# Performance work log

Measured on AMD Instinct MI355X. Metric: run time of the kernel, lower is better.

The kernel has to match this reference:

```python
import jax, jax.numpy as jnp
import numpy as np

N, CIN, C, COUT, K27, KNN_K = 65536, 1, 128, 128, 27, 16
C4, C2 = C // 4, C // 2


def _w(key, shape, fan_in):
    return (jax.random.normal(key, shape, dtype=jnp.float32) * (fan_in ** -0.5))


def setup_inputs() -> dict:
    key = jax.random.key(0)
    ks = jax.random.split(key, 32)
    inp = {
        "feats": jax.random.normal(ks[0], (N, CIN), dtype=jnp.float32),
        # kernel-map neighbor indices; value N means 'no neighbor at this offset'
        "nbr_idx": jax.random.randint(ks[1], (N, K27), 0, N + 1, dtype=jnp.int32),
        "knn_idx": jax.random.randint(ks[2], (N, KNN_K), 0, N, dtype=jnp.int32),
        "W_in": _w(ks[3], (K27, CIN, C), K27 * CIN), "b_in": jnp.zeros((C,), jnp.float32),
        "W_conv0": _w(ks[4], (3, K27, C, C), K27 * C), "b_conv0": jnp.zeros((3, C), jnp.float32),
        "W_conv1": _w(ks[5], (3, K27, C, C), K27 * C), "b_conv1": jnp.zeros((3, C), jnp.float32),
        "Wq": _w(ks[6], (3, C, C), C), "Wk": _w(ks[7], (3, C, C), C),
        "Wv": _w(ks[8], (3, C, C), C), "Wo": _w(ks[9], (3, C, C), C),
        "bo": jnp.zeros((3, C), jnp.float32),
        "W_a0": _w(ks[10], (3, C, C4), C), "b_a0": jnp.zeros((3, C4), jnp.float32),
        "W_a1": _w(ks[11], (3, K27, C4, C4), K27 * C4), "b_a1": jnp.zeros((3, C4), jnp.float32),
        "W_a2": _w(ks[12], (3, C4, C2), C4), "b_a2": jnp.zeros((3, C2), jnp.float32),
        "W_b0": _w(ks[13], (3, K27, C, C4), K27 * C), "b_b0": jnp.zeros((3, C4), jnp.float32),
        "W_b1": _w(ks[14], (3, K27, C4, C2), K27 * C4), "b_b1": jnp.zeros((3, C2), jnp.float32),
        "W_out": _w(ks[15], (K27, C, COUT), K27 * C), "b_out": jnp.zeros((COUT,), jnp.float32),
    }
    return inp


def sparse_conv(x, idx, W, b):
    # x: [N,Cin]; idx: [N,27] with pad value N -> zero feature
    xp = jnp.concatenate([x, jnp.zeros((1, x.shape[1]), x.dtype)], axis=0)
    g = xp[idx]  # [N,27,Cin]
    return jnp.einsum('nkc,kco->no', g, W) + b


def knn_attn(x, idx, Wq, Wk, Wv, Wo, bo):
    q = x @ Wq
    kf = x @ Wk
    vf = x @ Wv
    kn = kf[idx]  # [N,k,C]
    vn = vf[idx]
    logits = jnp.einsum('nc,nkc->nk', q, kn) * (x.shape[-1] ** -0.5)
    a = jax.nn.softmax(logits, axis=-1)
    agg = jnp.einsum('nk,nkc->nc', a, vn)
    return x + agg @ Wo + bo


def irn(x, idx, Wa0, ba0, Wa1, ba1, Wa2, ba2, Wb0, bb0, Wb1, bb1):
    r = jax.nn.relu
    h = r(x @ Wa0 + ba0)                      # 1x1 conv
    h = r(sparse_conv(h, idx, Wa1, ba1))       # 3x3x3
    out0 = r(h @ Wa2 + ba2)                    # 1x1 conv
    g = r(sparse_conv(x, idx, Wb0, bb0))
    out1 = r(sparse_conv(g, idx, Wb1, bb1))
    return jnp.concatenate([out0, out1], axis=-1) + x


def reference(feats, nbr_idx, knn_idx, W_in, b_in, W_conv0, b_conv0, W_conv1, b_conv1,
              Wq, Wk, Wv, Wo, bo, W_a0, b_a0, W_a1, b_a1, W_a2, b_a2,
              W_b0, b_b0, W_b1, b_b1, W_out, b_out):
    r = jax.nn.relu
    out = sparse_conv(feats, nbr_idx, W_in, b_in)
    for s in range(3):
        h = sparse_conv(out, nbr_idx, W_conv0[s], b_conv0[s])
        h = r(knn_attn(h, knn_idx, Wq[s], Wk[s], Wv[s], Wo[s], bo[s]))
        h = sparse_conv(h, nbr_idx, W_conv1[s], b_conv1[s])
        out = irn(h, nbr_idx, W_a0[s], b_a0[s], W_a1[s], b_a1[s], W_a2[s], b_a2[s],
                  W_b0[s], b_b0[s], W_b1[s], b_b1[s])
    return sparse_conv(out, nbr_idx, W_out, b_out)
```

## Files before the change

kernel.cpp:

```cpp
#include <hip/hip_runtime.h>
#include <stdint.h>

typedef unsigned short u16;
typedef __attribute__((ext_vector_type(8))) short bf16x8;
typedef __attribute__((ext_vector_type(4))) float f32x4;

#define NPTS 65536
#define NK27 27
#define KNN 16

__device__ __forceinline__ u16 f2b(float f) {
  union { float f; uint32_t u; } v; v.f = f;
  uint32_t r = (v.u + 0x7fffu + ((v.u >> 16) & 1u)) >> 16;
  return (u16)r;
}
__device__ __forceinline__ float b2f(u16 h) {
  union { uint32_t u; float f; } v; v.u = ((uint32_t)h) << 16; return v.f;
}

__global__ __launch_bounds__(256) void wtrans(const float* __restrict__ src, u16* __restrict__ dst,
                                              int G, int CI, int CO) {
  int id = blockIdx.x * 256 + threadIdx.x;
  int tot = G * CI * CO;
  if (id >= tot) return;
  int cpr = CI / 8;
  int swzb = (cpr < 8 ? cpr : 8) - 1;
  int g = id / (CI * CO);
  int r = id - g * (CI * CO);
  int co = r / CI;
  int cis = r - co * CI;
  int c = cis / 8, e = cis - c * 8;
  int ci = (c ^ (co & swzb)) * 8 + e;
  dst[id] = f2b(src[(size_t)g * CI * CO + (size_t)ci * CO + co]);
}

__global__ __launch_bounds__(256) void itrans(const int* __restrict__ nbr, int* __restrict__ out) {
  int id = blockIdx.x * 256 + threadIdx.x;
  int k = id >> 16;
  int n = id & (NPTS - 1);
  out[id] = nbr[n * NK27 + k];
}

__global__ void zero_pads(u16* a, u16* b, u16* c, u16* d, u16* e) {
  int t = threadIdx.x;
  if (t < 128) { a[t] = 0; b[t] = 0; c[t] = 0; }
  if (t < 32) { d[t] = 0; e[t] = 0; }
}

__global__ __launch_bounds__(256) void conv_in_k(const float* __restrict__ feats, const int* __restrict__ idx,
                                                 const float* __restrict__ W, const float* __restrict__ b,
                                                 u16* __restrict__ out) {
  int t = blockIdx.x * 256 + threadIdx.x;
  int n = t >> 7;
  int co = t & 127;
  float acc = b[co];
  for (int k = 0; k < NK27; ++k) {
    int m = idx[n * NK27 + k];
    float f = (m < NPTS) ? feats[m] : 0.0f;
    acc += f * W[k * 128 + co];
  }
  out[(size_t)n * 128 + co] = f2b(acc);
}

#define GLDS16(g, l)                                                                        \
  __builtin_amdgcn_global_load_lds((const __attribute__((address_space(1))) void*)(g),      \
                                   (__attribute__((address_space(3))) void*)(l), 16, 0, 0)

template<int CIN, int COUT, int NK, int EMODE, bool OUTF32>
__global__ __launch_bounds__(512, 2)
void sconv(const u16* __restrict__ x, const int* __restrict__ idxt,
           const u16* __restrict__ Wt, const float* __restrict__ bias,
           const u16* __restrict__ res, int res_stride,
           void* __restrict__ yout, int out_stride) {
  static_assert(NK == 1 || (NK & 1), "NK odd or 1");
  constexpr int BM = 256;
  constexpr int KK = CIN / 32;
  constexpr int CPR = CIN / 8;
  constexpr int SWZB = (CPR < 8 ? CPR : 8) - 1;
  constexpr int N_REP = COUT / 16;
  constexpr int M_REP = 2;
  constexpr int BSZ = COUT * CIN;
  constexpr int BCH = BSZ / 8;
  constexpr int BISS = (BCH + 511) / 512;

  __shared__ __attribute__((aligned(16))) u16 Bs[2][BSZ];

  const int tid = threadIdx.x;
  const int lane = tid & 63;
  const int wave = tid >> 6;
  const int n0 = blockIdx.x * BM;
  const int lr = lane & 15;
  const int lh = lane >> 4;
  const int row0 = wave * 32;

  f32x4 acc[M_REP][N_REP];
#pragma unroll
  for (int i = 0; i < M_REP; ++i)
#pragma unroll
    for (int j = 0; j < N_REP; ++j) acc[i][j] = (f32x4){0.f, 0.f, 0.f, 0.f};

  bf16x8 A0[M_REP][KK], A1[M_REP][KK];
  int mn[M_REP];

  auto stageB = [&](int k) {
    const u16* src = Wt + (size_t)k * BSZ;
    u16* dst = &Bs[k & 1][0];
#pragma unroll
    for (int i = 0; i < BISS; ++i) {
      int cb = i * 512 + wave * 64;
      if (BCH % 512 == 0 || cb < BCH)
        GLDS16(src + (size_t)(cb + lane) * 8, dst + (size_t)cb * 8);
    }
  };
  auto loadIdx = [&](int k, int (&m)[M_REP]) {
#pragma unroll
    for (int mr = 0; mr < M_REP; ++mr)
      m[mr] = idxt[(size_t)k * NPTS + n0 + row0 + mr * 16 + lr];
  };
  auto issueA = [&](const int (&m)[M_REP], bf16x8 (&dst)[M_REP][KK]) {
#pragma unroll
    for (int mr = 0; mr < M_REP; ++mr)
#pragma unroll
      for (int kk = 0; kk < KK; ++kk)
        dst[mr][kk] = *(const bf16x8*)(x + (size_t)m[mr] * CIN + kk * 32 + lh * 8);
  };
  auto compute = [&](int buf, const bf16x8 (&AR)[M_REP][KK]) {
#pragma unroll
    for (int kk = 0; kk < KK; ++kk) {
      bf16x8 b[N_REP];
      int pc = (kk * 4 + lh) ^ (lr & SWZB);
#pragma unroll
      for (int nr = 0; nr < N_REP; ++nr)
        b[nr] = *(const bf16x8*)(&Bs[buf][(nr * 16 + lr) * CIN + pc * 8]);
#pragma unroll
      for (int mr = 0; mr < M_REP; ++mr)
#pragma unroll
        for (int nr = 0; nr < N_REP; ++nr)
          acc[mr][nr] = __builtin_amdgcn_mfma_f32_16x16x32_bf16(AR[mr][kk], b[nr], acc[mr][nr], 0, 0, 0);
    }
  };

  {
    int m0[M_REP];
    if (NK == 1) {
#pragma unroll
      for (int mr = 0; mr < M_REP; ++mr) m0[mr] = n0 + row0 + mr * 16 + lr;
    } else {
      loadIdx(0, m0);
    }
    stageB(0);
    issueA(m0, A0);
    if (NK > 1) loadIdx(1, mn);
  }
  __syncthreads();

#define TAP(kv, AR, AW)                                                       \
  {                                                                           \
    const int k_ = (kv);                                                      \
    if (k_ + 1 < NK) {                                                        \
      stageB(k_ + 1);                                                         \
      issueA(mn, AW);                                                         \
      if (k_ + 2 < NK) loadIdx(k_ + 2, mn);                                   \
    }                                                                         \
    __builtin_amdgcn_sched_barrier(0);                                        \
    compute(k_ & 1, AR);                                                      \
    if (k_ + 1 < NK) __syncthreads();                                         \
  }

  if constexpr (NK == 1) {
    compute(0, A0);
  } else {
    int k = 0;
    for (; k + 2 < NK; k += 2) {
      TAP(k, A0, A1);
      TAP(k + 1, A1, A0);
    }
    TAP(k, A0, A1);
  }
#undef TAP

#pragma unroll
  for (int mr = 0; mr < M_REP; ++mr) {
#pragma unroll
    for (int nr = 0; nr < N_REP; ++nr) {
      int col = nr * 16 + lr;
      float bv = bias ? bias[col] : 0.0f;
#pragma unroll
      for (int j = 0; j < 4; ++j) {
        int n = n0 + row0 + mr * 16 + lh * 4 + j;
        float v = acc[mr][nr][j] + bv;
        if (EMODE == 1) v = fmaxf(v, 0.0f);
        else if (EMODE == 2) v = fmaxf(v + b2f(res[(size_t)n * res_stride + col]), 0.0f);
        else if (EMODE == 3) v = fmaxf(v, 0.0f) + b2f(res[(size_t)n * res_stride + col]);
        if (OUTF32) ((float*)yout)[(size_t)n * out_stride + col] = v;
        else ((u16*)yout)[(size_t)n * out_stride + col] = f2b(v);
      }
    }
  }
}

__global__ __launch_bounds__(256)
void attn_k(const u16* __restrict__ qb, const u16* __restrict__ kb,
            const u16* __restrict__ vb, const int* __restrict__ knn,
            u16* __restrict__ agg) {
  int n = (blockIdx.x * 256 + threadIdx.x) >> 6;
  int lane = threadIdx.x & 63;
  int c0 = lane * 2;
  uint32_t qp = *(const uint32_t*)(qb + (size_t)n * 128 + c0);
  float q0 = b2f((u16)(qp & 0xffff)), q1 = b2f((u16)(qp >> 16));
  float lg[KNN];
  int ms[KNN];
#pragma unroll
  for (int j = 0; j < KNN; ++j) {
    int m = knn[n * KNN + j];
    ms[j] = m;
    uint32_t kp = *(const uint32_t*)(kb + (size_t)m * 128 + c0);
    float p = q0 * b2f((u16)(kp & 0xffff)) + q1 * b2f((u16)(kp >> 16));
#pragma unroll
    for (int d = 1; d < 64; d <<= 1) p += __shfl_xor(p, d);
    lg[j] = p * 0.08838834764831845f;
  }
  float mx = lg[0];
#pragma unroll
  for (int j = 1; j < KNN; ++j) mx = fmaxf(mx, lg[j]);
  float s = 0.f, w[KNN];
#pragma unroll
  for (int j = 0; j < KNN; ++j) { w[j] = __expf(lg[j] - mx); s += w[j]; }
  float inv = 1.0f / s;
  float a0 = 0.f, a1 = 0.f;
#pragma unroll
  for (int j = 0; j < KNN; ++j) {
    uint32_t vp = *(const uint32_t*)(vb + (size_t)ms[j] * 128 + c0);
    a0 += w[j] * b2f((u16)(vp & 0xffff));
    a1 += w[j] * b2f((u16)(vp >> 16));
  }
  a0 *= inv; a1 *= inv;
  uint32_t op = (uint32_t)f2b(a0) | ((uint32_t)f2b(a1) << 16);
  *(uint32_t*)(agg + (size_t)n * 128 + c0) = op;
}

extern "C" void kernel_launch(void* const* d_in, const int* in_sizes, int n_in,
                              void* d_out, int out_size, void* d_ws, size_t ws_size,
                              hipStream_t stream) {
  (void)in_sizes; (void)n_in; (void)out_size; (void)ws_size;
  const float* feats = (const float*)d_in[0];
  const int*   nbr   = (const int*)d_in[1];
  const int*   knn   = (const int*)d_in[2];
  const float* W_in  = (const float*)d_in[3];
  const float* b_in  = (const float*)d_in[4];
  const float* W_c0  = (const float*)d_in[5];
  const float* b_c0  = (const float*)d_in[6];
  const float* W_c1  = (const float*)d_in[7];
  const float* b_c1  = (const float*)d_in[8];
  const float* Wq    = (const float*)d_in[9];
  const float* Wk    = (const float*)d_in[10];
  const float* Wv    = (const float*)d_in[11];
  const float* Wo    = (const float*)d_in[12];
  const float* bo    = (const float*)d_in[13];
  const float* Wa0   = (const float*)d_in[14];
  const float* ba0   = (const float*)d_in[15];
  const float* Wa1   = (const float*)d_in[16];
  const float* ba1   = (const float*)d_in[17];
  const float* Wa2   = (const float*)d_in[18];
  const float* ba2   = (const float*)d_in[19];
  const float* Wb0   = (const float*)d_in[20];
  const float* bb0   = (const float*)d_in[21];
  const float* Wb1   = (const float*)d_in[22];
  const float* bb1   = (const float*)d_in[23];
  const float* W_out = (const float*)d_in[24];
  const float* b_out = (const float*)d_in[25];

  char* ws = (char*)d_ws;
  size_t off = 0;
  auto alloc = [&](size_t bytes) { size_t r = off; off += (bytes + 255) & ~(size_t)255; return r; };

  u16* wt_c0  = (u16*)(ws + alloc((size_t)81 * 16384 * 2));
  u16* wt_c1  = (u16*)(ws + alloc((size_t)81 * 16384 * 2));
  u16* wt_q   = (u16*)(ws + alloc((size_t)3 * 16384 * 2));
  u16* wt_k   = (u16*)(ws + alloc((size_t)3 * 16384 * 2));
  u16* wt_v   = (u16*)(ws + alloc((size_t)3 * 16384 * 2));
  u16* wt_o   = (u16*)(ws + alloc((size_t)3 * 16384 * 2));
  u16* wt_a0  = (u16*)(ws + alloc((size_t)3 * 128 * 32 * 2));
  u16* wt_a1  = (u16*)(ws + alloc((size_t)81 * 32 * 32 * 2));
  u16* wt_a2  = (u16*)(ws + alloc((size_t)3 * 32 * 64 * 2));
  u16* wt_b0  = (u16*)(ws + alloc((size_t)81 * 128 * 32 * 2));
  u16* wt_b1  = (u16*)(ws + alloc((size_t)81 * 32 * 64 * 2));
  u16* wt_out = (u16*)(ws + alloc((size_t)27 * 16384 * 2));
  int* idx_t  = (int*)(ws + alloc((size_t)NK27 * NPTS * 4));

  u16* B0 = (u16*)(ws + alloc((size_t)(NPTS + 1) * 128 * 2));
  u16* B1 = (u16*)(ws + alloc((size_t)NPTS * 128 * 2));
  u16* KB = (u16*)(ws + alloc((size_t)(NPTS + 1) * 128 * 2));
  u16* VB = (u16*)(ws + alloc((size_t)(NPTS + 1) * 128 * 2));
  u16* QB = (u16*)(ws + alloc((size_t)NPTS * 128 * 2));
  u16* H1 = (u16*)(ws + alloc((size_t)(NPTS + 1) * 32 * 2));
  u16* HA = (u16*)(ws + alloc((size_t)NPTS * 32 * 2));
  u16* G  = (u16*)(ws + alloc((size_t)(NPTS + 1) * 32 * 2));
  u16* AGG = B0;
  u16* B2 = KB;
  u16* B3 = VB;

  auto TG = [](int tot) { return (tot + 255) / 256; };
  wtrans<<<TG(81 * 16384), 256, 0, stream>>>(W_c0, wt_c0, 81, 128, 128);
  wtrans<<<TG(81 * 16384), 256, 0, stream>>>(W_c1, wt_c1, 81, 128, 128);
  wtrans<<<TG(3 * 16384), 256, 0, stream>>>(Wq, wt_q, 3, 128, 128);
  wtrans<<<TG(3 * 16384), 256, 0, stream>>>(Wk, wt_k, 3, 128, 128);
  wtrans<<<TG(3 * 16384), 256, 0, stream>>>(Wv, wt_v, 3, 128, 128);
  wtrans<<<TG(3 * 16384), 256, 0, stream>>>(Wo, wt_o, 3, 128, 128);
  wtrans<<<TG(3 * 128 * 32), 256, 0, stream>>>(Wa0, wt_a0, 3, 128, 32);
  wtrans<<<TG(81 * 32 * 32), 256, 0, stream>>>(Wa1, wt_a1, 81, 32, 32);
  wtrans<<<TG(3 * 32 * 64), 256, 0, stream>>>(Wa2, wt_a2, 3, 32, 64);
  wtrans<<<TG(81 * 128 * 32), 256, 0, stream>>>(Wb0, wt_b0, 81, 128, 32);
  wtrans<<<TG(81 * 32 * 64), 256, 0, stream>>>(Wb1, wt_b1, 81, 32, 64);
  wtrans<<<TG(27 * 16384), 256, 0, stream>>>(W_out, wt_out, 27, 128, 128);
  itrans<<<NK27 * NPTS / 256, 256, 0, stream>>>(nbr, idx_t);

  zero_pads<<<1, 256, 0, stream>>>(B0 + (size_t)NPTS * 128, KB + (size_t)NPTS * 128,
                                   VB + (size_t)NPTS * 128, H1 + (size_t)NPTS * 32,
                                   G + (size_t)NPTS * 32);

  conv_in_k<<<NPTS * 128 / 256, 256, 0, stream>>>(feats, nbr, W_in, b_in, B0);

  const int GB = NPTS / 256;
  for (int s = 0; s < 3; ++s) {
    const u16* wc0 = wt_c0 + (size_t)s * 27 * 16384;
    const u16* wc1 = wt_c1 + (size_t)s * 27 * 16384;
    const u16* wqs = wt_q + (size_t)s * 16384;
    const u16* wks = wt_k + (size_t)s * 16384;
    const u16* wvs = wt_v + (size_t)s * 16384;
    const u16* wos = wt_o + (size_t)s * 16384;
    const u16* wa0 = wt_a0 + (size_t)s * 4096;
    const u16* wa1 = wt_a1 + (size_t)s * 27648;
    const u16* wa2 = wt_a2 + (size_t)s * 2048;
    const u16* wb0 = wt_b0 + (size_t)s * 110592;
    const u16* wb1 = wt_b1 + (size_t)s * 55296;

    sconv<128, 128, 27, 0, false><<<GB, 512, 0, stream>>>(B0, idx_t, wc0, b_c0 + s * 128, nullptr, 0, B1, 128);
    sconv<128, 128, 1, 0, false><<<GB, 512, 0, stream>>>(B1, nullptr, wqs, nullptr, nullptr, 0, QB, 128);
    sconv<128, 128, 1, 0, false><<<GB, 512, 0, stream>>>(B1, nullptr, wks, nullptr, nullptr, 0, KB, 128);
    sconv<128, 128, 1, 0, false><<<GB, 512, 0, stream>>>(B1, nullptr, wvs, nullptr, nullptr, 0, VB, 128);
    attn_k<<<NPTS / 4, 256, 0, stream>>>(QB, KB, VB, knn, AGG);
    sconv<128, 128, 1, 2, false><<<GB, 512, 0, stream>>>(AGG, nullptr, wos, bo + s * 128, B1, 128, B2, 128);
    sconv<128, 128, 27, 0, false><<<GB, 512, 0, stream>>>(B2, idx_t, wc1, b_c1 + s * 128, nullptr, 0, B3, 128);
    sconv<128, 32, 1, 1, false><<<GB, 512, 0, stream>>>(B3, nullptr, wa0, ba0 + s * 32, nullptr, 0, H1, 32);
    sconv<32, 32, 27, 1, false><<<GB, 512, 0, stream>>>(H1, idx_t, wa1, ba1 + s * 32, nullptr, 0, HA, 32);
    sconv<32, 64, 1, 3, false><<<GB, 512, 0, stream>>>(HA, nullptr, wa2, ba2 + s * 64, B3, 128, B0, 128);
    sconv<128, 32, 27, 1, false><<<GB, 512, 0, stream>>>(B3, idx_t, wb0, bb0 + s * 32, nullptr, 0, G, 32);
    sconv<32, 64, 27, 3, false><<<GB, 512, 0, stream>>>(G, idx_t, wb1, bb1 + s * 64, B3 + 64, 128, (void*)(B0 + 64), 128);
  }
  sconv<128, 128, 27, 0, true><<<GB, 512, 0, stream>>>(B0, idx_t, wt_out, b_out, nullptr, 0, d_out, 128);
}
```

Before: 1.388 ms.

## Split waves over output columns in sparse conv and run input conv on MFMA

The sparse-conv kernel's wave tiling changes so that for 128-wide outputs, waves split 2x4 over columns and rows rather than each wave covering all columns for 32 rows. This lowers per-wave accumulator registers and B-fragment loads, and may improve occupancy or scheduling. The scalar input conv is replaced by a gather kernel that builds a padded 27->32 bf16 matrix, followed by a 1x1 MFMA GEMM. The A-gather is also issued before the B staging within each tap. The cost is an extra kernel launch plus an intermediate buffer.

New measurement: 1.671 ms. 1.2x slower.

```diff
diff --git a/kernel.cpp b/kernel.cpp
--- a/kernel.cpp
+++ b/kernel.cpp
@@ -34,6 +34,27 @@
   dst[id] = f2b(src[(size_t)g * CI * CO + (size_t)ci * CO + co]);
 }
 
+__global__ __launch_bounds__(256) void wtrans_in(const float* __restrict__ W, u16* __restrict__ dst) {
+  int id = blockIdx.x * 256 + threadIdx.x;
+  if (id >= 128 * 32) return;
+  int co = id >> 5, cis = id & 31;
+  int c = cis >> 3, e = cis & 7;
+  int ci = ((c ^ (co & 3)) << 3) | e;
+  dst[id] = (ci < NK27) ? f2b(W[ci * 128 + co]) : (u16)0;
+}
+
+__global__ __launch_bounds__(256) void g27(const float* __restrict__ feats, const int* __restrict__ nbr,
+                                           u16* __restrict__ G) {
+  int id = blockIdx.x * 256 + threadIdx.x;
+  int n = id >> 5, j = id & 31;
+  u16 v = 0;
+  if (j < NK27) {
+    int m = nbr[n * NK27 + j];
+    if (m < NPTS) v = f2b(feats[m]);
+  }
+  G[id] = v;
+}
+
 __global__ __launch_bounds__(256) void itrans(const int* __restrict__ nbr, int* __restrict__ out) {
   int id = blockIdx.x * 256 + threadIdx.x;
   int k = id >> 16;
@@ -45,21 +66,6 @@
   int t = threadIdx.x;
   if (t < 128) { a[t] = 0; b[t] = 0; c[t] = 0; }
   if (t < 32) { d[t] = 0; e[t] = 0; }
-}
-
-__global__ __launch_bounds__(256) void conv_in_k(const float* __restrict__ feats, const int* __restrict__ idx,
-                                                 const float* __restrict__ W, const float* __restrict__ b,
-                                                 u16* __restrict__ out) {
-  int t = blockIdx.x * 256 + threadIdx.x;
-  int n = t >> 7;
-  int co = t & 127;
-  float acc = b[co];
-  for (int k = 0; k < NK27; ++k) {
-    int m = idx[n * NK27 + k];
-    float f = (m < NPTS) ? feats[m] : 0.0f;
-    acc += f * W[k * 128 + co];
-  }
-  out[(size_t)n * 128 + co] = f2b(acc);
 }
 
 #define GLDS16(g, l)                                                                        \
@@ -72,13 +78,16 @@
            const u16* __restrict__ Wt, const float* __restrict__ bias,
            const u16* __restrict__ res, int res_stride,
            void* __restrict__ yout, int out_stride) {
-  static_assert(NK == 1 || (NK & 1), "NK odd or 1");
   constexpr int BM = 256;
   constexpr int KK = CIN / 32;
   constexpr int CPR = CIN / 8;
   constexpr int SWZB = (CPR < 8 ? CPR : 8) - 1;
-  constexpr int N_REP = COUT / 16;
-  constexpr int M_REP = 2;
+  constexpr int WAVES_N = (COUT >= 128) ? 2 : 1;
+  constexpr int WN = COUT / WAVES_N;
+  constexpr int N_REP = WN / 16;
+  constexpr int WAVES_M = 8 / WAVES_N;
+  constexpr int WM = BM / WAVES_M;
+  constexpr int M_REP = WM / 16;
   constexpr int BSZ = COUT * CIN;
   constexpr int BCH = BSZ / 8;
   constexpr int BISS = (BCH + 511) / 512;
@@ -91,7 +100,10 @@
   const int n0 = blockIdx.x * BM;
   const int lr = lane & 15;
   const int lh = lane >> 4;
-  const int row0 = wave * 32;
+  const int wn = wave % WAVES_N;
+  const int wm = wave / WAVES_N;
+  const int row0 = wm * WM;
+  const int col0 = wn * WN;
 
   f32x4 acc[M_REP][N_REP];
 #pragma unroll
@@ -131,7 +143,7 @@
       int pc = (kk * 4 + lh) ^ (lr & SWZB);
 #pragma unroll
       for (int nr = 0; nr < N_REP; ++nr)
-        b[nr] = *(const bf16x8*)(&Bs[buf][(nr * 16 + lr) * CIN + pc * 8]);
+        b[nr] = *(const bf16x8*)(&Bs[buf][(size_t)(col0 + nr * 16 + lr) * CIN + pc * 8]);
 #pragma unroll
       for (int mr = 0; mr < M_REP; ++mr)
 #pragma unroll
@@ -158,12 +170,12 @@
   {                                                                           \
     const int k_ = (kv);                                                      \
     if (k_ + 1 < NK) {                                                        \
+      issueA(mn, AW);                                                         \
       stageB(k_ + 1);                                                         \
-      issueA(mn, AW);                                                         \
       if (k_ + 2 < NK) loadIdx(k_ + 2, mn);                                   \
     }                                                                         \
     __builtin_amdgcn_sched_barrier(0);                                        \
-    compute(k_ & 1, AR);                                                      \
+    compute((k_) & 1, AR);                                                    \
     if (k_ + 1 < NK) __syncthreads();                                         \
   }
 
@@ -183,7 +195,7 @@
   for (int mr = 0; mr < M_REP; ++mr) {
 #pragma unroll
     for (int nr = 0; nr < N_REP; ++nr) {
-      int col = nr * 16 + lr;
+      int col = col0 + nr * 16 + lr;
       float bv = bias ? bias[col] : 0.0f;
 #pragma unroll
       for (int j = 0; j < 4; ++j) {
@@ -286,7 +298,9 @@
   u16* wt_b0  = (u16*)(ws + alloc((size_t)81 * 128 * 32 * 2));
   u16* wt_b1  = (u16*)(ws + alloc((size_t)81 * 32 * 64 * 2));
   u16* wt_out = (u16*)(ws + alloc((size_t)27 * 16384 * 2));
+  u16* wt_in  = (u16*)(ws + alloc((size_t)128 * 32 * 2));
   int* idx_t  = (int*)(ws + alloc((size_t)NK27 * NPTS * 4));
+  u16* G27    = (u16*)(ws + alloc((size_t)NPTS * 32 * 2));
 
   u16* B0 = (u16*)(ws + alloc((size_t)(NPTS + 1) * 128 * 2));
   u16* B1 = (u16*)(ws + alloc((size_t)NPTS * 128 * 2));
@@ -313,13 +327,15 @@
   wtrans<<<TG(81 * 128 * 32), 256, 0, stream>>>(Wb0, wt_b0, 81, 128, 32);
   wtrans<<<TG(81 * 32 * 64), 256, 0, stream>>>(Wb1, wt_b1, 81, 32, 64);
   wtrans<<<TG(27 * 16384), 256, 0, stream>>>(W_out, wt_out, 27, 128, 128);
+  wtrans_in<<<TG(128 * 32), 256, 0, stream>>>(W_in, wt_in);
   itrans<<<NK27 * NPTS / 256, 256, 0, stream>>>(nbr, idx_t);
 
   zero_pads<<<1, 256, 0, stream>>>(B0 + (size_t)NPTS * 128, KB + (size_t)NPTS * 128,
                                    VB + (size_t)NPTS * 128, H1 + (size_t)NPTS * 32,
                                    G + (size_t)NPTS * 32);
 
-  conv_in_k<<<NPTS * 128 / 256, 256, 0, stream>>>(feats, nbr, W_in, b_in, B0);
+  g27<<<NPTS * 32 / 256, 256, 0, stream>>>(feats, nbr, G27);
+  sconv<32, 128, 1, 0, false><<<NPTS / 256, 512, 0, stream>>>(G27, nullptr, wt_in, b_in, nullptr, 0, B0, 128);
 
   const int GB = NPTS / 256;
   for (int s = 0; s < 3; ++s) {
@@ -344,7 +360,7 @@
     sconv<128, 128, 27, 0, false><<<GB, 512, 0, stream>>>(B2, idx_t, wc1, b_c1 + s * 128, nullptr, 0, B3, 128);
     sconv<128, 32, 1, 1, false><<<GB, 512, 0, stream>>>(B3, nullptr, wa0, ba0 + s * 32, nullptr, 0, H1, 32);
     sconv<32, 32, 27, 1, false><<<GB, 512, 0, stream>>>(H1, idx_t, wa1, ba1 + s * 32, nullptr, 0, HA, 32);
-    sconv<32, 64, 1, 3, false><<<GB, 512, 0, stream>>>(HA, nullptr, wa2, ba2 + s * 64, B3, 128, B0, 128);
+    sconv<32, 64, 1, 3, false><<<GB, 512, 0, stream>>>(HA, idx_t, wa2, ba2 + s * 64, B3, 128, B0, 128);
     sconv<128, 32, 27, 1, false><<<GB, 512, 0, stream>>>(B3, idx_t, wb0, bb0 + s * 32, nullptr, 0, G, 32);
     sconv<32, 64, 27, 3, false><<<GB, 512, 0, stream>>>(G, idx_t, wb1, bb1 + s * 64, B3 + 64, 128, (void*)(B0 + 64), 128);
   }
```
